# Performance work log

Hardware: AMD Instinct MI355X
Metric: run time of the kernel (lower is better)

Reference implementation:

```python
import jax, jax.numpy as jnp
import numpy as np


def setup_inputs() -> dict:
    key = jax.random.key(0)
    k1, k2 = jax.random.split(key)
    hidden = jax.random.normal(k1, (32, 4096, 768), dtype=jnp.float32)
    querys = jax.random.normal(k2, (1, 768), dtype=jnp.float32)
    return {"hidden": hidden, "querys": querys}


def reference(hidden, querys):
    # scores: [B, S] = hidden @ querys^T (single query)
    scores = jnp.einsum("bsh,qh->bsq", hidden, querys)[..., 0]  # [B, S]
    attn = jax.nn.softmax(scores, axis=-1)                      # [B, S]
    # weighted sum over sequence: [B, H]
    result = jnp.einsum("bs,bsh->bh", attn, hidden)
    return result
```

## Files before the change

kernel.cpp:

```cpp
#include <hip/hip_runtime.h>
#include <math.h>

#define BATCH 32
#define SEQ   4096
#define HID   768
#define HV4   (HID / 4)
#define CHUNKS 64
#define ROWS_PER_BLOCK (SEQ / CHUNKS)
#define NWAVES 4
#define TROWS 8
#define NT    (ROWS_PER_BLOCK / TROWS)
#define TILE_F4 (TROWS * HV4)
#define WAVE_F4 (TILE_F4 / NWAVES)
#define CALLS   (WAVE_F4 / 64)

typedef __attribute__((ext_vector_type(4))) float f4v;

__device__ __forceinline__ float dot4(f4v a, f4v b) {
  return a.x * b.x + a.y * b.y + a.z * b.z + a.w * b.w;
}

__device__ __forceinline__ void async_copy16(const f4v* g, f4v* l) {
  __builtin_amdgcn_global_load_lds(
      (const __attribute__((address_space(1))) void*)g,
      (__attribute__((address_space(3))) void*)l,
      16, 0, 0);
}

__global__ __launch_bounds__(256, 3)
void attn_pass1(const float* __restrict__ hidden,
                const float* __restrict__ q,
                float* __restrict__ m_ws,
                float* __restrict__ l_ws,
                float* __restrict__ o_ws) {
  __shared__ float lds[2][TROWS * HID];
  __shared__ float s_m[NWAVES], s_l[NWAVES];

  const int chunk = blockIdx.x;
  const int b     = blockIdx.y;
  const int tid   = threadIdx.x;
  const int wave  = tid >> 6;
  const int lane  = tid & 63;

  const f4v* q4 = reinterpret_cast<const f4v*>(q);
  const f4v qa = q4[lane];
  const f4v qb = q4[lane + 64];
  const f4v qc = q4[lane + 128];

  const f4v* gbase = reinterpret_cast<const f4v*>(hidden)
                   + ((size_t)b * SEQ + (size_t)chunk * ROWS_PER_BLOCK) * HV4;
  f4v* l0 = reinterpret_cast<f4v*>(lds[0]);
  f4v* l1 = reinterpret_cast<f4v*>(lds[1]);
  const int si = wave * WAVE_F4 + lane;

  #pragma unroll
  for (int c = 0; c < CALLS; ++c)
    async_copy16(gbase + 0 * TILE_F4 + si + c * 64, l0 + si + c * 64);
  #pragma unroll
  for (int c = 0; c < CALLS; ++c)
    async_copy16(gbase + 1 * TILE_F4 + si + c * 64, l1 + si + c * 64);

  float m = -INFINITY;
  float l = 0.0f;
  f4v oa = (f4v)0.0f;
  f4v ob = (f4v)0.0f;
  f4v oc = (f4v)0.0f;

  #pragma unroll
  for (int t = 0; t < NT; ++t) {
    f4v* lb = (t & 1) ? l1 : l0;

    __builtin_amdgcn_sched_barrier(0);
    if (t < NT - 1) asm volatile("s_waitcnt vmcnt(6)" ::: "memory");
    else            asm volatile("s_waitcnt vmcnt(0)" ::: "memory");
    __builtin_amdgcn_s_barrier();
    __builtin_amdgcn_sched_barrier(0);

    const f4v* r0 = lb + (size_t)(2 * wave + 0) * HV4;
    const f4v* r1 = lb + (size_t)(2 * wave + 1) * HV4;
    const f4v a0 = r0[lane], b0 = r0[lane + 64], c0 = r0[lane + 128];
    const f4v a1 = r1[lane], b1 = r1[lane + 64], c1 = r1[lane + 128];

    float p0 = dot4(a0, qa) + dot4(b0, qb) + dot4(c0, qc);
    float p1 = dot4(a1, qa) + dot4(b1, qb) + dot4(c1, qc);
    #pragma unroll
    for (int off = 32; off >= 1; off >>= 1) {
      p0 += __shfl_xor(p0, off, 64);
      p1 += __shfl_xor(p1, off, 64);
    }

    const float gm = fmaxf(p0, p1);
    if (gm > m) {
      const float a = __expf(m - gm);
      l *= a;
      oa *= a; ob *= a; oc *= a;
      m = gm;
    }
    const float e0 = __expf(p0 - m);
    const float e1 = __expf(p1 - m);
    l += e0 + e1;
    oa += e0 * a0 + e1 * a1;
    ob += e0 * b0 + e1 * b1;
    oc += e0 * c0 + e1 * c1;

    asm volatile("s_waitcnt lgkmcnt(0)" ::: "memory");
    __builtin_amdgcn_sched_barrier(0);
    __builtin_amdgcn_s_barrier();
    __builtin_amdgcn_sched_barrier(0);

    if (t + 2 < NT) {
      #pragma unroll
      for (int c = 0; c < CALLS; ++c)
        async_copy16(gbase + (size_t)(t + 2) * TILE_F4 + si + c * 64,
                     lb + si + c * 64);
    }
  }

  float (*s_o)[HID] = reinterpret_cast<float(*)[HID]>(lds[0]);
  f4v* so4 = reinterpret_cast<f4v*>(s_o[wave]);
  so4[lane]       = oa;
  so4[lane + 64]  = ob;
  so4[lane + 128] = oc;
  if (lane == 0) { s_m[wave] = m; s_l[wave] = l; }
  __syncthreads();

  const float mb = fmaxf(fmaxf(s_m[0], s_m[1]), fmaxf(s_m[2], s_m[3]));
  const float w0 = __expf(s_m[0] - mb);
  const float w1 = __expf(s_m[1] - mb);
  const float w2 = __expf(s_m[2] - mb);
  const float w3 = __expf(s_m[3] - mb);
  const float lsum = w0 * s_l[0] + w1 * s_l[1] + w2 * s_l[2] + w3 * s_l[3];

  const int pidx = b * CHUNKS + chunk;
  float* O = o_ws + (size_t)pidx * HID;
  #pragma unroll
  for (int j = 0; j < 3; ++j) {
    const int h = tid + 256 * j;
    O[h] = w0 * s_o[0][h] + w1 * s_o[1][h] + w2 * s_o[2][h] + w3 * s_o[3][h];
  }
  if (tid == 0) { m_ws[pidx] = mb; l_ws[pidx] = lsum; }
}

__global__ __launch_bounds__(128)
void attn_pass2(const float* __restrict__ m_ws,
                const float* __restrict__ l_ws,
                const float* __restrict__ o_ws,
                float* __restrict__ out) {
  const int b = blockIdx.x;
  const int h = blockIdx.y * 128 + threadIdx.x;

  float mg = -INFINITY;
  #pragma unroll 8
  for (int c = 0; c < CHUNKS; ++c)
    mg = fmaxf(mg, m_ws[b * CHUNKS + c]);

  float L = 0.0f;
  float acc = 0.0f;
  #pragma unroll 8
  for (int c = 0; c < CHUNKS; ++c) {
    const int pi = b * CHUNKS + c;
    const float a = __expf(m_ws[pi] - mg);
    L += a * l_ws[pi];
    acc += a * o_ws[(size_t)pi * HID + h];
  }
  out[(size_t)b * HID + h] = acc / L;
}

extern "C" void kernel_launch(void* const* d_in, const int* in_sizes, int n_in,
                              void* d_out, int out_size, void* d_ws, size_t ws_size,
                              hipStream_t stream) {
  const float* hidden = (const float*)d_in[0];
  const float* q      = (const float*)d_in[1];
  float* out = (float*)d_out;

  float* m_ws = (float*)d_ws;
  float* l_ws = m_ws + BATCH * CHUNKS;
  float* o_ws = l_ws + BATCH * CHUNKS;

  dim3 grid1(CHUNKS, BATCH);
  attn_pass1<<<grid1, 256, 0, stream>>>(hidden, q, m_ws, l_ws, o_ws);
  dim3 grid2(BATCH, HID / 128);
  attn_pass2<<<grid2, 128, 0, stream>>>(m_ws, l_ws, o_ws, out);
}
```

Baseline: 526.6 us.

## Give each wave a private LDS ring buffer to drop block barriers

Each wave now streams its own contiguous run of 16 rows through a private four-row LDS ring using async global-to-LDS copies. This removes the two block-wide s_barrier calls per tile, and the next row's copy is issued right after the current row's LDS reads. The cost is one row per iteration instead of two, so the shuffle-reduction chain is no longer amortised across two rows. LDS use also rises from 48KB to 48KB-equivalent per-wave rings, the same total, and a __syncthreads is added before the rings are reused for the cross-wave reduction.

```diff
diff --git a/kernel.cpp b/kernel.cpp
--- a/kernel.cpp
+++ b/kernel.cpp
@@ -8,11 +8,8 @@
 #define CHUNKS 64
 #define ROWS_PER_BLOCK (SEQ / CHUNKS)
 #define NWAVES 4
-#define TROWS 8
-#define NT    (ROWS_PER_BLOCK / TROWS)
-#define TILE_F4 (TROWS * HV4)
-#define WAVE_F4 (TILE_F4 / NWAVES)
-#define CALLS   (WAVE_F4 / 64)
+#define ROWS_PER_WAVE (ROWS_PER_BLOCK / NWAVES)
+#define RING 4
 
 typedef __attribute__((ext_vector_type(4))) float f4v;
 
@@ -27,13 +24,31 @@
       16, 0, 0);
 }
 
+__device__ __forceinline__ void stage_row(const f4v* gbase, f4v* ring,
+                                          int row, int lane) {
+  const f4v* g = gbase + (size_t)row * HV4;
+  f4v* dst = ring + (row & (RING - 1)) * HV4;
+  async_copy16(g + lane,       dst + lane);
+  async_copy16(g + lane + 64,  dst + lane + 64);
+  async_copy16(g + lane + 128, dst + lane + 128);
+}
+
+__device__ __forceinline__ void vwait(int n) {
+  switch (n) {
+    case 0: asm volatile("s_waitcnt vmcnt(0)" ::: "memory"); break;
+    case 3: asm volatile("s_waitcnt vmcnt(3)" ::: "memory"); break;
+    case 6: asm volatile("s_waitcnt vmcnt(6)" ::: "memory"); break;
+    default: asm volatile("s_waitcnt vmcnt(9)" ::: "memory"); break;
+  }
+}
+
 __global__ __launch_bounds__(256, 3)
 void attn_pass1(const float* __restrict__ hidden,
                 const float* __restrict__ q,
                 float* __restrict__ m_ws,
                 float* __restrict__ l_ws,
                 float* __restrict__ o_ws) {
-  __shared__ float lds[2][TROWS * HID];
+  __shared__ float lds[NWAVES][RING * HID];
   __shared__ float s_m[NWAVES], s_l[NWAVES];
 
   const int chunk = blockIdx.x;
@@ -47,18 +62,13 @@
   const f4v qb = q4[lane + 64];
   const f4v qc = q4[lane + 128];
 
+  const int row0 = chunk * ROWS_PER_BLOCK + wave * ROWS_PER_WAVE;
   const f4v* gbase = reinterpret_cast<const f4v*>(hidden)
-                   + ((size_t)b * SEQ + (size_t)chunk * ROWS_PER_BLOCK) * HV4;
-  f4v* l0 = reinterpret_cast<f4v*>(lds[0]);
-  f4v* l1 = reinterpret_cast<f4v*>(lds[1]);
-  const int si = wave * WAVE_F4 + lane;
+                   + ((size_t)b * SEQ + (size_t)row0) * HV4;
+  f4v* ring = reinterpret_cast<f4v*>(lds[wave]);
 
   #pragma unroll
-  for (int c = 0; c < CALLS; ++c)
-    async_copy16(gbase + 0 * TILE_F4 + si + c * 64, l0 + si + c * 64);
-  #pragma unroll
-  for (int c = 0; c < CALLS; ++c)
-    async_copy16(gbase + 1 * TILE_F4 + si + c * 64, l1 + si + c * 64);
+  for (int r = 0; r < RING; ++r) stage_row(gbase, ring, r, lane);
 
   float m = -INFINITY;
   float l = 0.0f;
@@ -67,55 +77,38 @@
   f4v oc = (f4v)0.0f;
 
   #pragma unroll
-  for (int t = 0; t < NT; ++t) {
-    f4v* lb = (t & 1) ? l1 : l0;
-
-    __builtin_amdgcn_sched_barrier(0);
-    if (t < NT - 1) asm volatile("s_waitcnt vmcnt(6)" ::: "memory");
-    else            asm volatile("s_waitcnt vmcnt(0)" ::: "memory");
-    __builtin_amdgcn_s_barrier();
+  for (int r = 0; r < ROWS_PER_WAVE; ++r) {
+    vwait(r <= 12 ? 9 : 3 * (15 - r));
     __builtin_amdgcn_sched_barrier(0);
 
-    const f4v* r0 = lb + (size_t)(2 * wave + 0) * HV4;
-    const f4v* r1 = lb + (size_t)(2 * wave + 1) * HV4;
-    const f4v a0 = r0[lane], b0 = r0[lane + 64], c0 = r0[lane + 128];
-    const f4v a1 = r1[lane], b1 = r1[lane + 64], c1 = r1[lane + 128];
-
-    float p0 = dot4(a0, qa) + dot4(b0, qb) + dot4(c0, qc);
-    float p1 = dot4(a1, qa) + dot4(b1, qb) + dot4(c1, qc);
-    #pragma unroll
-    for (int off = 32; off >= 1; off >>= 1) {
-      p0 += __shfl_xor(p0, off, 64);
-      p1 += __shfl_xor(p1, off, 64);
-    }
-
-    const float gm = fmaxf(p0, p1);
-    if (gm > m) {
-      const float a = __expf(m - gm);
-      l *= a;
-      oa *= a; ob *= a; oc *= a;
-      m = gm;
-    }
-    const float e0 = __expf(p0 - m);
-    const float e1 = __expf(p1 - m);
-    l += e0 + e1;
-    oa += e0 * a0 + e1 * a1;
-    ob += e0 * b0 + e1 * b1;
-    oc += e0 * c0 + e1 * c1;
+    const f4v* rp = ring + (r & (RING - 1)) * HV4;
+    const f4v a0 = rp[lane];
+    const f4v b0 = rp[lane + 64];
+    const f4v c0 = rp[lane + 128];
 
     asm volatile("s_waitcnt lgkmcnt(0)" ::: "memory");
     __builtin_amdgcn_sched_barrier(0);
-    __builtin_amdgcn_s_barrier();
-    __builtin_amdgcn_sched_barrier(0);
+    if (r + RING < ROWS_PER_WAVE) stage_row(gbase, ring, r + RING, lane);
 
-    if (t + 2 < NT) {
-      #pragma unroll
-      for (int c = 0; c < CALLS; ++c)
-        async_copy16(gbase + (size_t)(t + 2) * TILE_F4 + si + c * 64,
-                     lb + si + c * 64);
+    float p = dot4(a0, qa) + dot4(b0, qb) + dot4(c0, qc);
+    #pragma unroll
+    for (int off = 32; off >= 1; off >>= 1)
+      p += __shfl_xor(p, off, 64);
+
+    if (p > m) {
+      const float s = __expf(m - p);
+      l *= s;
+      oa *= s; ob *= s; oc *= s;
+      m = p;
     }
+    const float e = __expf(p - m);
+    l += e;
+    oa += e * a0;
+    ob += e * b0;
+    oc += e * c0;
   }
 
+  __syncthreads();
   float (*s_o)[HID] = reinterpret_cast<float(*)[HID]>(lds[0]);
   f4v* so4 = reinterpret_cast<f4v*>(s_o[wave]);
   so4[lane]       = oa;
```

After: 526.8 us. About the same (+0.0%).
